# Kernel tuning notes

Measured on AMD Instinct MI355X. Metric: run time of the kernel, lower is better.

The kernel has to match this reference:

```python
import jax, jax.numpy as jnp
import numpy as np

N, P, E, H = 64, 1024, 512, 8
R = E // H  # head dim


def _xavier(key, shape, dtype=jnp.float32):
    fan_in, fan_out = shape[-1], shape[-2] if len(shape) > 1 else shape[-1]
    lim = jnp.sqrt(6.0 / (fan_in + fan_out)).astype(dtype)
    return jax.random.uniform(key, shape, dtype, -lim, lim)


def setup_inputs() -> dict:
    key = jax.random.key(0)
    k1, k2, k3, k4 = jax.random.split(key, 4)
    x = jax.random.normal(k1, (N, P, E), dtype=jnp.float32)
    alpha = _xavier(k2, (H, P))          # translation-invariant attention weights
    V = _xavier(k3, (H, R, E))           # per-head value projection
    W = _xavier(k4, (E, E))              # Dense kernel
    b = jnp.zeros((E,), dtype=jnp.float32)  # Dense bias
    return {"x": x, "alpha": alpha, "V": V, "W": W, "b": b}


def _log_cosh(x):
    # log(cosh(x)) = |x| + log1p(exp(-2|x|)) - log(2), numerically stable
    ax = jnp.abs(x)
    return ax + jnp.log1p(jnp.exp(-2.0 * ax)) - jnp.log(2.0).astype(x.dtype)


def reference(x, alpha, V, W, b):
    n, p, e = x.shape
    # circulant matrix: alpha_mat[h, i, j] = alpha[h, (j - i) mod P]
    # (equivalent to stacking jnp.roll(alpha, shift=i) over i)
    idx = (jnp.arange(p)[None, :] - jnp.arange(p)[:, None]) % p  # (P, P)
    alpha_mat = alpha[:, idx]                                    # (H, P, P)
    ws = jnp.einsum('hrd,npd->nhpr', V, x)                       # (N, H, P, R)
    y = jnp.einsum('hpj,nhjr->nphr', alpha_mat, ws)              # (N, P, H, R)
    y = y.reshape(n, p, -1)                                      # (N, P, E)
    y = y @ W + b
    return _log_cosh(y)
```

## Files before the change

kernel.cpp:

```cpp
#include <hip/hip_runtime.h>
#include <math.h>

typedef float f32x4 __attribute__((ext_vector_type(4)));
typedef __bf16 bf16x8 __attribute__((ext_vector_type(8)));
typedef unsigned short u16x8 __attribute__((ext_vector_type(8)));
typedef unsigned short u16x4 __attribute__((ext_vector_type(4)));

#define LN2F_ 0.69314718055994530942f

__device__ inline unsigned short f2bf(float f) {
    unsigned u = __builtin_bit_cast(unsigned, f);
    u += 0x7fffu + ((u >> 16) & 1u);
    return (unsigned short)(u >> 16);
}

__device__ inline bf16x8 frag_ld(const unsigned short* Ls, int s, int ml, int q) {
    return __builtin_bit_cast(bf16x8,
        *(const u16x8*)(Ls + s * 512 + (((q) << 4) + (ml ^ ((q) << 1))) * 8));
}

__device__ inline void gll16(const unsigned short* g, unsigned short* l) {
    __builtin_amdgcn_global_load_lds(
        (const __attribute__((address_space(1))) unsigned int*)g,
        (__attribute__((address_space(3))) unsigned int*)l, 16, 0, 0);
}

__global__ __launch_bounds__(256) void k_cvt(const float* __restrict__ in,
                                             unsigned short* __restrict__ out, int n4) {
    int i = blockIdx.x * 256 + threadIdx.x;
    if (i >= n4) return;
    float4 v = ((const float4*)in)[i];
    u16x4 o = { f2bf(v.x), f2bf(v.y), f2bf(v.z), f2bf(v.w) };
    *(u16x4*)(out + (size_t)i * 4) = o;
}

__global__ __launch_bounds__(256) void k_build_am(const float* __restrict__ alpha,
                                                  unsigned short* __restrict__ am) {
    int t = blockIdx.x * 256 + threadIdx.x;
    int j8 = (t & 127) << 3;
    int p  = (t >> 7) & 1023;
    int h  = t >> 17;
    const float* ar = alpha + (h << 10);
    u16x8 o;
#pragma unroll
    for (int q = 0; q < 8; ++q) o[q] = f2bf(ar[(j8 + q - p) & 1023]);
    *(u16x8*)(am + ((size_t)t << 3)) = o;
}

__global__ __launch_bounds__(256) void k_build_wt(const float* __restrict__ W,
                                                  unsigned short* __restrict__ WT) {
    int t = blockIdx.x * 256 + threadIdx.x;
    int e1 = t >> 9, e = t & 511;
    WT[t] = f2bf(W[e * 512 + e1]);
}

__global__ __launch_bounds__(256) void k_gemm1(const unsigned short* __restrict__ A,
                                               const unsigned short* __restrict__ B,
                                               unsigned short* __restrict__ wsT) {
    __shared__ __align__(16) unsigned short As[2][128 * 32];
    __shared__ __align__(16) unsigned short Bs[2][128 * 32];
    const int tid = threadIdx.x;
    const int flat = blockIdx.x;
    const int xcd = flat & 7, slot = flat >> 3;
    const int m0 = (xcd * 64 + (slot >> 2)) * 128;
    const int e0 = (slot & 3) * 128;
    const int w = tid >> 6, lane = tid & 63, ml = lane & 15, quad = lane >> 4;
    const int wr = w >> 1, wc = w & 1;
    const int srl = (lane & 15) ^ ((lane >> 4) << 1);
    const int scl = lane >> 4;
    const unsigned short* pA0 = A + (size_t)(m0 + w * 32 + srl) * 512 + scl * 8;
    const unsigned short* pA1 = pA0 + 16 * 512;
    const unsigned short* pB0 = B + (size_t)(e0 + w * 32 + srl) * 512 + scl * 8;
    const unsigned short* pB1 = pB0 + 16 * 512;
    auto STAGE = [&](int b, int ko) {
        gll16(pA0 + ko, As[b] + w * 1024);
        gll16(pA1 + ko, As[b] + w * 1024 + 512);
        gll16(pB0 + ko, Bs[b] + w * 1024);
        gll16(pB1 + ko, Bs[b] + w * 1024 + 512);
    };
    f32x4 acc[4][4] = {};
    STAGE(0, 0);
    __syncthreads();
#pragma unroll 2
    for (int k = 0; k < 16; ++k) {
        const int cur = k & 1;
        if (k < 15) STAGE(cur ^ 1, (k + 1) * 32);
        bf16x8 af[4], bfr[4];
#pragma unroll
        for (int i = 0; i < 4; ++i) {
            af[i]  = frag_ld(As[cur], wr * 4 + i, ml, quad);
            bfr[i] = frag_ld(Bs[cur], wc * 4 + i, ml, quad);
        }
        __builtin_amdgcn_s_setprio(1);
#pragma unroll
        for (int i = 0; i < 4; ++i)
#pragma unroll
            for (int j = 0; j < 4; ++j)
                acc[i][j] = __builtin_amdgcn_mfma_f32_16x16x32_bf16(af[i], bfr[j], acc[i][j], 0, 0, 0);
        __builtin_amdgcn_s_setprio(0);
        __syncthreads();
    }
    const int n = m0 >> 10;
    const int pblk = m0 & 1023;
#pragma unroll
    for (int i = 0; i < 4; ++i) {
        int p = pblk + wr * 64 + i * 16 + quad * 4;
#pragma unroll
        for (int j = 0; j < 4; ++j) {
            int e = e0 + wc * 64 + j * 16 + ml;
            u16x4 o = { f2bf(acc[i][j][0]), f2bf(acc[i][j][1]),
                        f2bf(acc[i][j][2]), f2bf(acc[i][j][3]) };
            *(u16x4*)(wsT + ((size_t)n * 512 + e) * 1024 + p) = o;
        }
    }
}

__global__ __launch_bounds__(512) void k_gemm2(const unsigned short* __restrict__ wsT,
                                               const unsigned short* __restrict__ am,
                                               unsigned short* __restrict__ y) {
    __shared__ __align__(16) unsigned short As[2][256 * 32];
    __shared__ __align__(16) unsigned short Bs[2][128 * 32];
    const int tid = threadIdx.x;
    const int flat = blockIdx.x;
    const int xcd = flat & 7, slot = flat >> 3;
    const int panel = xcd * 16 + (slot >> 3);
    const int p0 = (slot & 7) * 128;
    const int h  = panel & 7;
    const int n0 = (panel >> 3) * 4;
    const int w = tid >> 6, lane = tid & 63, ml = lane & 15, quad = lane >> 4;
    const int wn = w >> 1, wp = w & 1;
    const int srl = (lane & 15) ^ ((lane >> 4) << 1);
    const int scl = lane >> 4;
    const unsigned short* pA0 = wsT + (size_t)(n0 + (w >> 1)) * 524288
        + (size_t)(h * 64 + ((2 * w) & 3) * 16 + srl) * 1024 + scl * 8;
    const unsigned short* pA1 = wsT + (size_t)(n0 + (w >> 1)) * 524288
        + (size_t)(h * 64 + ((2 * w + 1) & 3) * 16 + srl) * 1024 + scl * 8;
    const unsigned short* pB = am + ((size_t)h * 1024 + p0 + w * 16 + srl) * 1024 + scl * 8;
    auto STAGE = [&](int b, int jo) {
        gll16(pA0 + jo, As[b] + (2 * w) * 512);
        gll16(pA1 + jo, As[b] + (2 * w) * 512 + 512);
        gll16(pB + jo, Bs[b] + w * 512);
    };
    f32x4 acc[4][4] = {};
    STAGE(0, 0);
    __syncthreads();
#pragma unroll 2
    for (int k = 0; k < 32; ++k) {
        const int cur = k & 1;
        if (k < 31) STAGE(cur ^ 1, (k + 1) * 32);
        bf16x8 af[4], bfr[4];
#pragma unroll
        for (int mt = 0; mt < 4; ++mt)
            af[mt] = frag_ld(As[cur], wn * 4 + mt, ml, quad);
#pragma unroll
        for (int nt = 0; nt < 4; ++nt)
            bfr[nt] = frag_ld(Bs[cur], wp * 4 + nt, ml, quad);
        __builtin_amdgcn_s_setprio(1);
#pragma unroll
        for (int mt = 0; mt < 4; ++mt)
#pragma unroll
            for (int nt = 0; nt < 4; ++nt)
                acc[mt][nt] = __builtin_amdgcn_mfma_f32_16x16x32_bf16(af[mt], bfr[nt], acc[mt][nt], 0, 0, 0);
        __builtin_amdgcn_s_setprio(0);
        __syncthreads();
    }
    const int n = n0 + wn;
#pragma unroll
    for (int mt = 0; mt < 4; ++mt) {
        int r0 = mt * 16 + quad * 4;
#pragma unroll
        for (int nt = 0; nt < 4; ++nt) {
            int p = p0 + wp * 64 + nt * 16 + ml;
            u16x4 o = { f2bf(acc[mt][nt][0]), f2bf(acc[mt][nt][1]),
                        f2bf(acc[mt][nt][2]), f2bf(acc[mt][nt][3]) };
            *(u16x4*)(y + ((size_t)n * 1024 + p) * 512 + h * 64 + r0) = o;
        }
    }
}

__global__ __launch_bounds__(256) void k_gemm3(const unsigned short* __restrict__ A,
                                               const unsigned short* __restrict__ B,
                                               const float* __restrict__ bias,
                                               float* __restrict__ out) {
    __shared__ __align__(16) unsigned short As[2][128 * 32];
    __shared__ __align__(16) unsigned short Bs[2][128 * 32];
    const int tid = threadIdx.x;
    const int flat = blockIdx.x;
    const int xcd = flat & 7, slot = flat >> 3;
    const int m0 = (xcd * 64 + (slot >> 2)) * 128;
    const int e0 = (slot & 3) * 128;
    const int w = tid >> 6, lane = tid & 63, ml = lane & 15, quad = lane >> 4;
    const int wr = w >> 1, wc = w & 1;
    const int srl = (lane & 15) ^ ((lane >> 4) << 1);
    const int scl = lane >> 4;
    const unsigned short* pA0 = A + (size_t)(m0 + w * 32 + srl) * 512 + scl * 8;
    const unsigned short* pA1 = pA0 + 16 * 512;
    const unsigned short* pB0 = B + (size_t)(e0 + w * 32 + srl) * 512 + scl * 8;
    const unsigned short* pB1 = pB0 + 16 * 512;
    auto STAGE = [&](int b, int ko) {
        gll16(pA0 + ko, As[b] + w * 1024);
        gll16(pA1 + ko, As[b] + w * 1024 + 512);
        gll16(pB0 + ko, Bs[b] + w * 1024);
        gll16(pB1 + ko, Bs[b] + w * 1024 + 512);
    };
    f32x4 acc[4][4] = {};
    STAGE(0, 0);
    __syncthreads();
#pragma unroll 2
    for (int k = 0; k < 16; ++k) {
        const int cur = k & 1;
        if (k < 15) STAGE(cur ^ 1, (k + 1) * 32);
        bf16x8 af[4], bfr[4];
#pragma unroll
        for (int i = 0; i < 4; ++i) {
            af[i]  = frag_ld(As[cur], wr * 4 + i, ml, quad);
            bfr[i] = frag_ld(Bs[cur], wc * 4 + i, ml, quad);
        }
        __builtin_amdgcn_s_setprio(1);
#pragma unroll
        for (int i = 0; i < 4; ++i)
#pragma unroll
            for (int j = 0; j < 4; ++j)
                acc[i][j] = __builtin_amdgcn_mfma_f32_16x16x32_bf16(af[i], bfr[j], acc[i][j], 0, 0, 0);
        __builtin_amdgcn_s_setprio(0);
        __syncthreads();
    }
#pragma unroll
    for (int j = 0; j < 4; ++j) {
        int e = e0 + wc * 64 + j * 16 + ml;
        float bv = bias[e];
#pragma unroll
        for (int i = 0; i < 4; ++i) {
            int mg = m0 + wr * 64 + i * 16 + quad * 4;
#pragma unroll
            for (int r = 0; r < 4; ++r) {
                float v  = acc[i][j][r] + bv;
                float ax = fabsf(v);
                float t  = __expf(-2.0f * ax);
                out[(size_t)(mg + r) * 512 + e] = ax + __logf(1.0f + t) - LN2F_;
            }
        }
    }
}

extern "C" void kernel_launch(void* const* d_in, const int* in_sizes, int n_in,
                              void* d_out, int out_size, void* d_ws, size_t ws_size,
                              hipStream_t stream) {
    const float* x     = (const float*)d_in[0];
    const float* alpha = (const float*)d_in[1];
    const float* V     = (const float*)d_in[2];
    const float* W     = (const float*)d_in[3];
    const float* b     = (const float*)d_in[4];

    unsigned short* am  = (unsigned short*)d_out;
    unsigned short* Vb  = am + 8388608;
    unsigned short* Xb  = Vb + 262144;
    unsigned short* wsT = (unsigned short*)d_ws;
    unsigned short* y   = wsT + 33554432;
    unsigned short* WT  = wsT;
    float* out = (float*)d_out;

    k_cvt<<<256, 256, 0, stream>>>(V, Vb, 65536);
    k_cvt<<<32768, 256, 0, stream>>>(x, Xb, 8388608);
    k_build_am<<<4096, 256, 0, stream>>>(alpha, am);

    k_gemm1<<<dim3(2048), 256, 0, stream>>>(Xb, Vb, wsT);
    k_gemm2<<<dim3(1024), 512, 0, stream>>>(wsT, am, y);
    k_build_wt<<<1024, 256, 0, stream>>>(W, WT);
    k_gemm3<<<dim3(2048), 256, 0, stream>>>(y, WT, b, out);
}
```

Before: 500.9 us.

## Triple-buffer LDS staging in all three GEMMs with vmcnt-based waits

Each GEMM kernel moves from double-buffered to triple-buffered LDS tiles, issuing loads two K-steps ahead. The per-iteration __syncthreads after compute is replaced by one s_waitcnt vmcnt(N) plus s_barrier at the top of each iteration. The goal is to hide global-to-LDS latency and cut barrier count per step. In exchange LDS use per block grows by half, which may lower occupancy, and the barrier placement must still keep the buffer being overwritten from being read.

```diff
diff --git a/kernel.cpp b/kernel.cpp
--- a/kernel.cpp
+++ b/kernel.cpp
@@ -54,11 +54,16 @@
     WT[t] = f2bf(W[e * 512 + e1]);
 }
 
+#define PIPE_SYNC(N)                                        \
+    asm volatile("s_waitcnt vmcnt(" #N ")" ::: "memory");   \
+    __builtin_amdgcn_s_barrier();                           \
+    __builtin_amdgcn_sched_barrier(0);
+
 __global__ __launch_bounds__(256) void k_gemm1(const unsigned short* __restrict__ A,
                                                const unsigned short* __restrict__ B,
                                                unsigned short* __restrict__ wsT) {
-    __shared__ __align__(16) unsigned short As[2][128 * 32];
-    __shared__ __align__(16) unsigned short Bs[2][128 * 32];
+    __shared__ __align__(16) unsigned short As[3][128 * 32];
+    __shared__ __align__(16) unsigned short Bs[3][128 * 32];
     const int tid = threadIdx.x;
     const int flat = blockIdx.x;
     const int xcd = flat & 7, slot = flat >> 3;
@@ -79,12 +84,7 @@
         gll16(pB1 + ko, Bs[b] + w * 1024 + 512);
     };
     f32x4 acc[4][4] = {};
-    STAGE(0, 0);
-    __syncthreads();
-#pragma unroll 2
-    for (int k = 0; k < 16; ++k) {
-        const int cur = k & 1;
-        if (k < 15) STAGE(cur ^ 1, (k + 1) * 32);
+    auto COMPUTE = [&](int cur) {
         bf16x8 af[4], bfr[4];
 #pragma unroll
         for (int i = 0; i < 4; ++i) {
@@ -98,8 +98,16 @@
             for (int j = 0; j < 4; ++j)
                 acc[i][j] = __builtin_amdgcn_mfma_f32_16x16x32_bf16(af[i], bfr[j], acc[i][j], 0, 0, 0);
         __builtin_amdgcn_s_setprio(0);
-        __syncthreads();
-    }
+    };
+    STAGE(0, 0);
+    STAGE(1, 32);
+    for (int k = 0; k < 15; ++k) {
+        PIPE_SYNC(4)
+        if (k < 14) STAGE((k + 2) % 3, (k + 2) * 32);
+        COMPUTE(k % 3);
+    }
+    PIPE_SYNC(0)
+    COMPUTE(0);
     const int n = m0 >> 10;
     const int pblk = m0 & 1023;
 #pragma unroll
@@ -118,8 +126,8 @@
 __global__ __launch_bounds__(512) void k_gemm2(const unsigned short* __restrict__ wsT,
                                                const unsigned short* __restrict__ am,
                                                unsigned short* __restrict__ y) {
-    __shared__ __align__(16) unsigned short As[2][256 * 32];
-    __shared__ __align__(16) unsigned short Bs[2][128 * 32];
+    __shared__ __align__(16) unsigned short As[3][256 * 32];
+    __shared__ __align__(16) unsigned short Bs[3][128 * 32];
     const int tid = threadIdx.x;
     const int flat = blockIdx.x;
     const int xcd = flat & 7, slot = flat >> 3;
@@ -142,12 +150,7 @@
         gll16(pB + jo, Bs[b] + w * 512);
     };
     f32x4 acc[4][4] = {};
-    STAGE(0, 0);
-    __syncthreads();
-#pragma unroll 2
-    for (int k = 0; k < 32; ++k) {
-        const int cur = k & 1;
-        if (k < 31) STAGE(cur ^ 1, (k + 1) * 32);
+    auto COMPUTE = [&](int cur) {
         bf16x8 af[4], bfr[4];
 #pragma unroll
         for (int mt = 0; mt < 4; ++mt)
@@ -162,8 +165,16 @@
             for (int nt = 0; nt < 4; ++nt)
                 acc[mt][nt] = __builtin_amdgcn_mfma_f32_16x16x32_bf16(af[mt], bfr[nt], acc[mt][nt], 0, 0, 0);
         __builtin_amdgcn_s_setprio(0);
-        __syncthreads();
-    }
+    };
+    STAGE(0, 0);
+    STAGE(1, 32);
+    for (int k = 0; k < 31; ++k) {
+        PIPE_SYNC(3)
+        if (k < 30) STAGE((k + 2) % 3, (k + 2) * 32);
+        COMPUTE(k % 3);
+    }
+    PIPE_SYNC(0)
+    COMPUTE(1);
     const int n = n0 + wn;
 #pragma unroll
     for (int mt = 0; mt < 4; ++mt) {
@@ -182,8 +193,8 @@
                                                const unsigned short* __restrict__ B,
                                                const float* __restrict__ bias,
                                                float* __restrict__ out) {
-    __shared__ __align__(16) unsigned short As[2][128 * 32];
-    __shared__ __align__(16) unsigned short Bs[2][128 * 32];
+    __shared__ __align__(16) unsigned short As[3][128 * 32];
+    __shared__ __align__(16) unsigned short Bs[3][128 * 32];
     const int tid = threadIdx.x;
     const int flat = blockIdx.x;
     const int xcd = flat & 7, slot = flat >> 3;
@@ -204,12 +215,7 @@
         gll16(pB1 + ko, Bs[b] + w * 1024 + 512);
     };
     f32x4 acc[4][4] = {};
-    STAGE(0, 0);
-    __syncthreads();
-#pragma unroll 2
-    for (int k = 0; k < 16; ++k) {
-        const int cur = k & 1;
-        if (k < 15) STAGE(cur ^ 1, (k + 1) * 32);
+    auto COMPUTE = [&](int cur) {
         bf16x8 af[4], bfr[4];
 #pragma unroll
         for (int i = 0; i < 4; ++i) {
@@ -223,8 +229,16 @@
             for (int j = 0; j < 4; ++j)
                 acc[i][j] = __builtin_amdgcn_mfma_f32_16x16x32_bf16(af[i], bfr[j], acc[i][j], 0, 0, 0);
         __builtin_amdgcn_s_setprio(0);
-        __syncthreads();
-    }
+    };
+    STAGE(0, 0);
+    STAGE(1, 32);
+    for (int k = 0; k < 15; ++k) {
+        PIPE_SYNC(4)
+        if (k < 14) STAGE((k + 2) % 3, (k + 2) * 32);
+        COMPUTE(k % 3);
+    }
+    PIPE_SYNC(0)
+    COMPUTE(0);
 #pragma unroll
     for (int j = 0; j < 4; ++j) {
         int e = e0 + wc * 64 + j * 16 + ml;
```

Result: no change. 498.9 us (-0.4%).

## Load MFMA fragments directly from global memory into registers, bypassing LDS

Applied to the files above, without the earlier changes.

All three GEMM kernels drop LDS double buffering with global_load_lds and barriers. Each wave now loads its bf16 fragments straight from global memory into registers, using a two-set register ping-pong. This removes the LDS traffic and the __syncthreads per k-step. In exchange, data shared between waves is no longer reused through LDS, so redundant global/L2 loads rise and the access pattern is less coalesced.

```diff
diff --git a/kernel.cpp b/kernel.cpp
--- a/kernel.cpp
+++ b/kernel.cpp
@@ -12,17 +12,6 @@
     unsigned u = __builtin_bit_cast(unsigned, f);
     u += 0x7fffu + ((u >> 16) & 1u);
     return (unsigned short)(u >> 16);
-}
-
-__device__ inline bf16x8 frag_ld(const unsigned short* Ls, int s, int ml, int q) {
-    return __builtin_bit_cast(bf16x8,
-        *(const u16x8*)(Ls + s * 512 + (((q) << 4) + (ml ^ ((q) << 1))) * 8));
-}
-
-__device__ inline void gll16(const unsigned short* g, unsigned short* l) {
-    __builtin_amdgcn_global_load_lds(
-        (const __attribute__((address_space(1))) unsigned int*)g,
-        (__attribute__((address_space(3))) unsigned int*)l, 16, 0, 0);
 }
 
 __global__ __launch_bounds__(256) void k_cvt(const float* __restrict__ in,
@@ -54,11 +43,10 @@
     WT[t] = f2bf(W[e * 512 + e1]);
 }
 
+
 __global__ __launch_bounds__(256) void k_gemm1(const unsigned short* __restrict__ A,
                                                const unsigned short* __restrict__ B,
                                                unsigned short* __restrict__ wsT) {
-    __shared__ __align__(16) unsigned short As[2][128 * 32];
-    __shared__ __align__(16) unsigned short Bs[2][128 * 32];
     const int tid = threadIdx.x;
     const int flat = blockIdx.x;
     const int xcd = flat & 7, slot = flat >> 3;
@@ -66,39 +54,34 @@
     const int e0 = (slot & 3) * 128;
     const int w = tid >> 6, lane = tid & 63, ml = lane & 15, quad = lane >> 4;
     const int wr = w >> 1, wc = w & 1;
-    const int srl = (lane & 15) ^ ((lane >> 4) << 1);
-    const int scl = lane >> 4;
-    const unsigned short* pA0 = A + (size_t)(m0 + w * 32 + srl) * 512 + scl * 8;
-    const unsigned short* pA1 = pA0 + 16 * 512;
-    const unsigned short* pB0 = B + (size_t)(e0 + w * 32 + srl) * 512 + scl * 8;
-    const unsigned short* pB1 = pB0 + 16 * 512;
-    auto STAGE = [&](int b, int ko) {
-        gll16(pA0 + ko, As[b] + w * 1024);
-        gll16(pA1 + ko, As[b] + w * 1024 + 512);
-        gll16(pB0 + ko, Bs[b] + w * 1024);
-        gll16(pB1 + ko, Bs[b] + w * 1024 + 512);
-    };
+    const unsigned short* pa = A + (size_t)(m0 + wr * 64 + ml) * 512 + quad * 8;
+    const unsigned short* pb = B + (size_t)(e0 + wc * 64 + ml) * 512 + quad * 8;
     f32x4 acc[4][4] = {};
-    STAGE(0, 0);
-    __syncthreads();
-#pragma unroll 2
-    for (int k = 0; k < 16; ++k) {
-        const int cur = k & 1;
-        if (k < 15) STAGE(cur ^ 1, (k + 1) * 32);
-        bf16x8 af[4], bfr[4];
-#pragma unroll
-        for (int i = 0; i < 4; ++i) {
-            af[i]  = frag_ld(As[cur], wr * 4 + i, ml, quad);
-            bfr[i] = frag_ld(Bs[cur], wc * 4 + i, ml, quad);
-        }
+    u16x8 aE[4], bE[4], aO[4], bO[4];
+    auto LOAD = [&](u16x8* ar, u16x8* br, int ko) {
+#pragma unroll
+        for (int i = 0; i < 4; ++i) {
+            ar[i] = *(const u16x8*)(pa + (size_t)i * 8192 + ko);
+            br[i] = *(const u16x8*)(pb + (size_t)i * 8192 + ko);
+        }
+    };
+    auto MF = [&](u16x8* ar, u16x8* br) {
         __builtin_amdgcn_s_setprio(1);
 #pragma unroll
         for (int i = 0; i < 4; ++i)
 #pragma unroll
             for (int j = 0; j < 4; ++j)
-                acc[i][j] = __builtin_amdgcn_mfma_f32_16x16x32_bf16(af[i], bfr[j], acc[i][j], 0, 0, 0);
+                acc[i][j] = __builtin_amdgcn_mfma_f32_16x16x32_bf16(
+                    __builtin_bit_cast(bf16x8, ar[i]),
+                    __builtin_bit_cast(bf16x8, br[j]), acc[i][j], 0, 0, 0);
         __builtin_amdgcn_s_setprio(0);
-        __syncthreads();
+    };
+    LOAD(aE, bE, 0);
+    for (int k0 = 0; k0 < 512; k0 += 64) {
+        if (k0 + 32 < 512) LOAD(aO, bO, k0 + 32);
+        MF(aE, bE);
+        if (k0 + 64 < 512) LOAD(aE, bE, k0 + 64);
+        MF(aO, bO);
     }
     const int n = m0 >> 10;
     const int pblk = m0 & 1023;
@@ -118,8 +101,6 @@
 __global__ __launch_bounds__(512) void k_gemm2(const unsigned short* __restrict__ wsT,
                                                const unsigned short* __restrict__ am,
                                                unsigned short* __restrict__ y) {
-    __shared__ __align__(16) unsigned short As[2][256 * 32];
-    __shared__ __align__(16) unsigned short Bs[2][128 * 32];
     const int tid = threadIdx.x;
     const int flat = blockIdx.x;
     const int xcd = flat & 7, slot = flat >> 3;
@@ -129,40 +110,35 @@
     const int n0 = (panel >> 3) * 4;
     const int w = tid >> 6, lane = tid & 63, ml = lane & 15, quad = lane >> 4;
     const int wn = w >> 1, wp = w & 1;
-    const int srl = (lane & 15) ^ ((lane >> 4) << 1);
-    const int scl = lane >> 4;
-    const unsigned short* pA0 = wsT + (size_t)(n0 + (w >> 1)) * 524288
-        + (size_t)(h * 64 + ((2 * w) & 3) * 16 + srl) * 1024 + scl * 8;
-    const unsigned short* pA1 = wsT + (size_t)(n0 + (w >> 1)) * 524288
-        + (size_t)(h * 64 + ((2 * w + 1) & 3) * 16 + srl) * 1024 + scl * 8;
-    const unsigned short* pB = am + ((size_t)h * 1024 + p0 + w * 16 + srl) * 1024 + scl * 8;
-    auto STAGE = [&](int b, int jo) {
-        gll16(pA0 + jo, As[b] + (2 * w) * 512);
-        gll16(pA1 + jo, As[b] + (2 * w) * 512 + 512);
-        gll16(pB + jo, Bs[b] + w * 512);
-    };
+    const unsigned short* pa = wsT + (size_t)(n0 + wn) * 524288
+                                   + (size_t)(h * 64 + ml) * 1024 + quad * 8;
+    const unsigned short* pb = am + ((size_t)h * 1024 + p0 + wp * 64 + ml) * 1024 + quad * 8;
     f32x4 acc[4][4] = {};
-    STAGE(0, 0);
-    __syncthreads();
-#pragma unroll 2
-    for (int k = 0; k < 32; ++k) {
-        const int cur = k & 1;
-        if (k < 31) STAGE(cur ^ 1, (k + 1) * 32);
-        bf16x8 af[4], bfr[4];
+    u16x8 aE[4], bE[4], aO[4], bO[4];
+    auto LOAD = [&](u16x8* ar, u16x8* br, int ko) {
+#pragma unroll
+        for (int i = 0; i < 4; ++i) {
+            ar[i] = *(const u16x8*)(pa + (size_t)i * 16384 + ko);
+            br[i] = *(const u16x8*)(pb + (size_t)i * 16384 + ko);
+        }
+    };
+    auto MF = [&](u16x8* ar, u16x8* br) {
+        __builtin_amdgcn_s_setprio(1);
 #pragma unroll
         for (int mt = 0; mt < 4; ++mt)
-            af[mt] = frag_ld(As[cur], wn * 4 + mt, ml, quad);
-#pragma unroll
-        for (int nt = 0; nt < 4; ++nt)
-            bfr[nt] = frag_ld(Bs[cur], wp * 4 + nt, ml, quad);
-        __builtin_amdgcn_s_setprio(1);
-#pragma unroll
-        for (int mt = 0; mt < 4; ++mt)
 #pragma unroll
             for (int nt = 0; nt < 4; ++nt)
-                acc[mt][nt] = __builtin_amdgcn_mfma_f32_16x16x32_bf16(af[mt], bfr[nt], acc[mt][nt], 0, 0, 0);
+                acc[mt][nt] = __builtin_amdgcn_mfma_f32_16x16x32_bf16(
+                    __builtin_bit_cast(bf16x8, ar[mt]),
+                    __builtin_bit_cast(bf16x8, br[nt]), acc[mt][nt], 0, 0, 0);
         __builtin_amdgcn_s_setprio(0);
-        __syncthreads();
+    };
+    LOAD(aE, bE, 0);
+    for (int k0 = 0; k0 < 1024; k0 += 64) {
+        if (k0 + 32 < 1024) LOAD(aO, bO, k0 + 32);
+        MF(aE, bE);
+        if (k0 + 64 < 1024) LOAD(aE, bE, k0 + 64);
+        MF(aO, bO);
     }
     const int n = n0 + wn;
 #pragma unroll
@@ -182,8 +158,6 @@
                                                const unsigned short* __restrict__ B,
                                                const float* __restrict__ bias,
                                                float* __restrict__ out) {
-    __shared__ __align__(16) unsigned short As[2][128 * 32];
-    __shared__ __align__(16) unsigned short Bs[2][128 * 32];
     const int tid = threadIdx.x;
     const int flat = blockIdx.x;
     const int xcd = flat & 7, slot = flat >> 3;
@@ -191,39 +165,34 @@
     const int e0 = (slot & 3) * 128;
     const int w = tid >> 6, lane = tid & 63, ml = lane & 15, quad = lane >> 4;
     const int wr = w >> 1, wc = w & 1;
-    const int srl = (lane & 15) ^ ((lane >> 4) << 1);
-    const int scl = lane >> 4;
-    const unsigned short* pA0 = A + (size_t)(m0 + w * 32 + srl) * 512 + scl * 8;
-    const unsigned short* pA1 = pA0 + 16 * 512;
-    const unsigned short* pB0 = B + (size_t)(e0 + w * 32 + srl) * 512 + scl * 8;
-    const unsigned short* pB1 = pB0 + 16 * 512;
-    auto STAGE = [&](int b, int ko) {
-        gll16(pA0 + ko, As[b] + w * 1024);
-        gll16(pA1 + ko, As[b] + w * 1024 + 512);
-        gll16(pB0 + ko, Bs[b] + w * 1024);
-        gll16(pB1 + ko, Bs[b] + w * 1024 + 512);
-    };
+    const unsigned short* pa = A + (size_t)(m0 + wr * 64 + ml) * 512 + quad * 8;
+    const unsigned short* pb = B + (size_t)(e0 + wc * 64 + ml) * 512 + quad * 8;
     f32x4 acc[4][4] = {};
-    STAGE(0, 0);
-    __syncthreads();
-#pragma unroll 2
-    for (int k = 0; k < 16; ++k) {
-        const int cur = k & 1;
-        if (k < 15) STAGE(cur ^ 1, (k + 1) * 32);
-        bf16x8 af[4], bfr[4];
-#pragma unroll
-        for (int i = 0; i < 4; ++i) {
-            af[i]  = frag_ld(As[cur], wr * 4 + i, ml, quad);
-            bfr[i] = frag_ld(Bs[cur], wc * 4 + i, ml, quad);
-        }
+    u16x8 aE[4], bE[4], aO[4], bO[4];
+    auto LOAD = [&](u16x8* ar, u16x8* br, int ko) {
+#pragma unroll
+        for (int i = 0; i < 4; ++i) {
+            ar[i] = *(const u16x8*)(pa + (size_t)i * 8192 + ko);
+            br[i] = *(const u16x8*)(pb + (size_t)i * 8192 + ko);
+        }
+    };
+    auto MF = [&](u16x8* ar, u16x8* br) {
         __builtin_amdgcn_s_setprio(1);
 #pragma unroll
         for (int i = 0; i < 4; ++i)
 #pragma unroll
             for (int j = 0; j < 4; ++j)
-                acc[i][j] = __builtin_amdgcn_mfma_f32_16x16x32_bf16(af[i], bfr[j], acc[i][j], 0, 0, 0);
+                acc[i][j] = __builtin_amdgcn_mfma_f32_16x16x32_bf16(
+                    __builtin_bit_cast(bf16x8, ar[i]),
+                    __builtin_bit_cast(bf16x8, br[j]), acc[i][j], 0, 0, 0);
         __builtin_amdgcn_s_setprio(0);
-        __syncthreads();
+    };
+    LOAD(aE, bE, 0);
+    for (int k0 = 0; k0 < 512; k0 += 64) {
+        if (k0 + 32 < 512) LOAD(aO, bO, k0 + 32);
+        MF(aE, bE);
+        if (k0 + 64 < 512) LOAD(aE, bE, k0 + 64);
+        MF(aO, bO);
     }
 #pragma unroll
     for (int j = 0; j < 4; ++j) {
```

After: 722.1 us. 1.44x slower.
